# Performance work log

Hardware: AMD Instinct MI355X
Metric: run time of the kernel (lower is better)

The kernel has to match this reference:

```python
import jax, jax.numpy as jnp
import numpy as np

BS, L, S, AMB = 64, 64, 63, 32   # batch, sentence len, opseq steps, ambiguities per step
H, E, V, MLP = 128, 300, 50000, 1024
EPS = 1e-8


def setup_inputs() -> dict:
    key = jax.random.key(0)
    ks = jax.random.split(key, 12)
    u = lambda k, shp: jax.random.uniform(k, shp, dtype=jnp.float32) * 0.1
    return {
        "sentences1": jax.random.randint(ks[0], (BS, L), 0, V, dtype=jnp.int32),
        "operations1": jax.random.randint(ks[1], (BS, S, 2 * AMB), 0, L, dtype=jnp.int32),
        "oopl1": jnp.full((BS,), L + S, dtype=jnp.int32),
        "sentences2": jax.random.randint(ks[2], (BS, L), 0, V, dtype=jnp.int32),
        "operations2": jax.random.randint(ks[3], (BS, S, 2 * AMB), 0, L, dtype=jnp.int32),
        "oopl2": jnp.full((BS,), L + S, dtype=jnp.int32),
        "W": u(ks[4], (5 * H, E)),
        "U": u(ks[5], (5 * H, 2 * H)),
        "b": jnp.zeros((5 * H,), dtype=jnp.float32),
        "energy_u": u(ks[6], (H,)),
        "unk_embedding": u(ks[7], (E,)),
        "word_embeddings": jax.random.normal(ks[8], (V, E), dtype=jnp.float32),
        "A": u(ks[9], (MLP, 4 * H)),
        "a": u(ks[10], (MLP,)),
        "inv_temperature": jnp.float32(1.0),
    }


def _gates(preact, ccL, ccR):
    # preact: [..., 5H]; tree-LSTM cell (i, fL, fR, o, u gates)
    i = jax.nn.sigmoid(preact[..., :H])
    fL = jax.nn.sigmoid(preact[..., H:2 * H])
    fR = jax.nn.sigmoid(preact[..., 2 * H:3 * H])
    o = jax.nn.sigmoid(preact[..., 3 * H:4 * H])
    u = jnp.tanh(preact[..., 4 * H:5 * H])
    c = fL * ccL + fR * ccR + i * u
    h = o * jnp.tanh(c)
    return c, h


def _run_chart(sentences, operations, W, U, b, energy_u, unk_embedding,
               word_embeddings, inv_temperature):
    bs = sentences.shape[0]
    # leaf phase: embed each word, preact = W @ emb + b, ccL = ccR = 0
    emb = jnp.where(sentences[..., None] >= 0,
                    word_embeddings[jnp.clip(sentences, 0)], unk_embedding)  # [bs,L,E]
    preact = jnp.einsum('ble,ge->blg', emb, W) + b                            # [bs,L,5H]
    c, h = _gates(preact, 0.0, 0.0)
    chart = jnp.zeros((bs, L + S, 2 * H), dtype=jnp.float32)
    chart = chart.at[:, :L, :].set(jnp.concatenate([c, h], axis=-1))

    def step(chart, inp):
        ops, pos = inp                                   # ops: [bs, 2*AMB], pos: scalar
        entries = jnp.take_along_axis(chart, ops[:, :, None].astype(jnp.int32), axis=1)
        entries = entries.reshape(bs, AMB, 2, 2 * H)     # [bs, amb, (L,R), 2H]
        ccL = entries[:, :, 0, :H]
        ccR = entries[:, :, 1, :H]
        hh = entries[:, :, :, H:].reshape(bs, AMB, 2 * H)  # concat(hL, hR)
        pre = jnp.einsum('bak,gk->bag', hh, U) + b         # [bs, amb, 5H]
        c, h = _gates(pre, ccL, ccR)
        # cosine similarity of h against energy_u
        hn = jnp.maximum(jnp.sqrt(jnp.sum(h * h, axis=-1)), EPS)
        un = jnp.maximum(jnp.sqrt(jnp.sum(energy_u * energy_u)), EPS)
        e = jnp.einsum('bah,h->ba', h, energy_u) / (hn * un)
        s = jax.nn.softmax(e * inv_temperature, axis=1)    # [bs, amb]
        combined = jnp.concatenate([jnp.einsum('ba,bah->bh', s, c),
                                    jnp.einsum('ba,bah->bh', s, h)], axis=-1)
        chart = jax.lax.dynamic_update_slice(chart, combined[:, None, :], (0, pos, 0))
        return chart, None

    ops_seq = jnp.swapaxes(operations, 0, 1)             # [S, bs, 2*AMB]
    positions = L + jnp.arange(S, dtype=jnp.int32)
    chart, _ = jax.lax.scan(step, chart, (ops_seq, positions))
    return chart


def reference(sentences1, operations1, oopl1, sentences2, operations2, oopl2,
              W, U, b, energy_u, unk_embedding, word_embeddings, A, a,
              inv_temperature):
    chart1 = _run_chart(sentences1, operations1, W, U, b, energy_u,
                        unk_embedding, word_embeddings, inv_temperature)
    chart2 = _run_chart(sentences2, operations2, W, U, b, energy_u,
                        unk_embedding, word_embeddings, inv_temperature)
    bs = chart1.shape[0]
    bidx = jnp.arange(bs)
    s1 = chart1[bidx, oopl1 - 1, H:]                     # final composed h, [bs, H]
    s2 = chart2[bidx, oopl2 - 1, H:]
    u = (s1 - s2) ** 2
    v = s1 * s2
    conc = jnp.concatenate([u, v, s1, s2], axis=1)       # [bs, 4H]
    out = jax.nn.relu(jnp.einsum('jk,ik->ij', A, conc) + a)
    return out
```

## Files before the change

kernel.cpp:

```cpp
#include <hip/hip_runtime.h>
#include <hip/hip_bf16.h>

#define BSZ 64
#define LL  64
#define SS  63
#define AMB 32
#define HH  128
#define EE  300
#define MLPN 1024
#define GG  640
#define K2  256
#define PP  127

typedef __attribute__((ext_vector_type(8))) short short8;
typedef __attribute__((ext_vector_type(4))) float f32x4;

__device__ __forceinline__ float sigf(float x) { return 1.f / (1.f + __expf(-x)); }

__device__ __forceinline__ unsigned short f2bf(float x) {
    unsigned int u = __float_as_uint(x);
    u += 0x7fffu + ((u >> 16) & 1u);
    return (unsigned short)(u >> 16);
}

#define PW 25600
#define PU 20480
__global__ void __launch_bounds__(256) prep_kernel(
        const float* __restrict__ W, const float* __restrict__ U,
        short* __restrict__ WTB, short* __restrict__ UTB) {
    int idx = blockIdx.x * 256 + threadIdx.x;
    if (idx < PW) {
        int lane = idx & 63, r = idx >> 6;
        int kk = r % 10, n = r / 10;
        int g = n * 16 + (lane & 15);
        int k0 = kk * 32 + ((lane >> 4) << 3);
        const float* src = W + (size_t)g * EE + k0;
        float f[8];
        if (k0 + 8 <= EE) {
            f32x4 x0 = *(const f32x4*)src;
            f32x4 x1 = *(const f32x4*)(src + 4);
            f[0]=x0[0]; f[1]=x0[1]; f[2]=x0[2]; f[3]=x0[3];
            f[4]=x1[0]; f[5]=x1[1]; f[6]=x1[2]; f[7]=x1[3];
        } else {
#pragma unroll
            for (int j = 0; j < 8; ++j) f[j] = (k0 + j < EE) ? src[j] : 0.f;
        }
        short8 v;
#pragma unroll
        for (int j = 0; j < 8; ++j) v[j] = (short)f2bf(f[j]);
        *(short8*)(WTB + (size_t)idx * 8) = v;
    } else if (idx < PW + PU) {
        int o = idx - PW;
        int lane = o & 63, r = o >> 6;
        int kk = r & 7, n = r >> 3;
        int g = n * 16 + (lane & 15);
        int k0 = kk * 32 + ((lane >> 4) << 3);
        const float* src = U + (size_t)g * K2 + k0;
        f32x4 x0 = *(const f32x4*)src;
        f32x4 x1 = *(const f32x4*)(src + 4);
        short8 v;
        v[0]=(short)f2bf(x0[0]); v[1]=(short)f2bf(x0[1]); v[2]=(short)f2bf(x0[2]); v[3]=(short)f2bf(x0[3]);
        v[4]=(short)f2bf(x1[0]); v[5]=(short)f2bf(x1[1]); v[6]=(short)f2bf(x1[2]); v[7]=(short)f2bf(x1[3]);
        *(short8*)(UTB + (size_t)o * 8) = v;
    }
}

__global__ void __launch_bounds__(1024) main_kernel(
        const int* __restrict__ sent1, const int* __restrict__ sent2,
        const int* __restrict__ ops1, const int* __restrict__ ops2,
        const int* __restrict__ oopl1, const int* __restrict__ oopl2,
        const short* __restrict__ WTB, const short* __restrict__ UTB,
        const float* __restrict__ bias, const float* __restrict__ eu,
        const float* __restrict__ invt,
        const float* __restrict__ unk, const float* __restrict__ wemb,
        float* __restrict__ chart) {
    __shared__ short8 As[40 * 64];
    __shared__ float chh[32][132];
    __shared__ float comb[2][2][HH];
    __shared__ int ops_lds[64];
    __shared__ float e_num[AMB], h2s[AMB], s_w[AMB];
    __shared__ int live_list[SS];
    __shared__ int nl_sh;
    __shared__ float un_sh;

    const int tid = threadIdx.x;
    const int pair = blockIdx.x;
    const int ch = pair >> 6, b = pair & 63;
    const int* sent = ch ? sent2 : sent1;
    const int* ops  = ch ? ops2 : ops1;
    const int* oopl = ch ? oopl2 : oopl1;
    float* chbase = chart + (size_t)pair * PP * K2;
    const float it = invt[0];
    const int w = tid >> 6, lane = tid & 63, quad = lane >> 4, l15 = lane & 15;

    if (tid < 64) {
        float v = eu[tid] * eu[tid] + eu[tid + 64] * eu[tid + 64];
        for (int off = 32; off >= 1; off >>= 1) v += __shfl_xor(v, off);
        if (tid == 0) un_sh = fmaxf(sqrtf(v), 1e-8f);

        unsigned long long mask = 0ull;
        int q0 = oopl[b] - 1 - LL;
        if (q0 >= 0) { if (q0 > SS - 1) q0 = SS - 1; mask = 1ull << q0; }
        for (int t = SS - 1; t >= 1; --t) {
            if (mask & (1ull << t)) {
                int p = ops[(b * SS + t) * 64 + tid];
                int q = p - LL;
                unsigned long long bit = (q >= 0 && q < t) ? (1ull << q) : 0ull;
                for (int off = 32; off >= 1; off >>= 1) bit |= __shfl_xor(bit, off);
                mask |= bit;
            }
        }
        if (tid == 0) {
            int n = 0;
            for (int t = 0; t < SS; ++t)
                if (mask & (1ull << t)) live_list[n++] = t;
            nl_sh = n;
        }
    }

#pragma unroll
    for (int i = 0; i < 3; ++i) {
        int slot = i * 1024 + tid;
        if (slot < 2560) {
            int t = slot / 40, oct = slot - t * 40;
            int s = sent[b * LL + t];
            const float* src = (s >= 0) ? (wemb + (size_t)s * EE) : unk;
            int k0 = oct * 8;
            float f[8];
            if (k0 + 8 <= EE) {
                f32x4 x0 = *(const f32x4*)(src + k0);
                f32x4 x1 = *(const f32x4*)(src + k0 + 4);
                f[0]=x0[0]; f[1]=x0[1]; f[2]=x0[2]; f[3]=x0[3];
                f[4]=x1[0]; f[5]=x1[1]; f[6]=x1[2]; f[7]=x1[3];
            } else {
#pragma unroll
                for (int j = 0; j < 8; ++j) f[j] = (k0 + j < EE) ? src[k0 + j] : 0.f;
            }
            short8 v;
#pragma unroll
            for (int j = 0; j < 8; ++j) v[j] = (short)f2bf(f[j]);
            As[((t >> 4) * 10 + (oct >> 2)) * 64 + ((oct & 3) << 4) + (t & 15)] = v;
        }
    }
#pragma unroll
    for (int i = 0; i < 4; ++i) {
        int off = i * 4096 + tid * 4;
        if (off < SS * K2) {
            f32x4 z = {0.f, 0.f, 0.f, 0.f};
            *(f32x4*)(chbase + (size_t)LL * K2 + off) = z;
        }
    }
    __syncthreads();

    {
        const int mt = w & 3, nug = w >> 2;
        f32x4 acc[2][3] = {};
        for (int kk = 0; kk < 10; ++kk) {
            short8 a0 = As[(mt * 10 + kk) * 64 + lane];
#pragma unroll
            for (int si = 0; si < 3; ++si) {
                int s5 = (si == 0) ? 0 : (si == 1 ? 3 : 4);
#pragma unroll
                for (int hf = 0; hf < 2; ++hf) {
                    int n = (nug + hf * 4) + 8 * s5;
                    short8 bv = *(const short8*)(WTB + ((size_t)(n * 10 + kk) * 64 + lane) * 8);
                    acc[hf][si] = __builtin_amdgcn_mfma_f32_16x16x32_bf16(a0, bv, acc[hf][si], 0, 0, 0);
                }
            }
        }
#pragma unroll
        for (int hf = 0; hf < 2; ++hf) {
            int jc = (nug + hf * 4) * 16 + l15;
            float bi = bias[jc], bo = bias[3 * HH + jc], bu = bias[4 * HH + jc];
#pragma unroll
            for (int r = 0; r < 4; ++r) {
                float pi = acc[hf][0][r] + bi;
                float po = acc[hf][1][r] + bo;
                float pu = acc[hf][2][r] + bu;
                float cv = sigf(pi) * tanhf(pu);
                float hv = sigf(po) * tanhf(cv);
                int l = mt * 16 + quad * 4 + r;
                chbase[(size_t)l * K2 + jc]      = cv;
                chbase[(size_t)l * K2 + HH + jc] = hv;
            }
        }
    }
    __syncthreads();

    const int nl = nl_sh;
    const float eul = eu[lane], euh = eu[64 + lane];
    const int smt = w & 1, snu = w >> 1;
    const int sjc = snu * 16 + l15;
    const float bi  = bias[sjc],          bfl = bias[HH + sjc];
    const float bfr = bias[2 * HH + sjc], bo  = bias[3 * HH + sjc];
    const float bu  = bias[4 * HH + sjc];

    for (int sidx = 0; sidx < nl; ++sidx) {
        const int t = live_list[sidx];
        if (tid < 64) ops_lds[tid] = min(max(ops[(b * SS + t) * 64 + tid], 0), PP - 1);
        __syncthreads();

        {
            int a = tid >> 5, oct = tid & 31, side = oct >> 4, m8 = oct & 15;
            const float* src = chbase + (size_t)ops_lds[2 * a + side] * K2 + HH + m8 * 8;
            f32x4 x0 = *(const f32x4*)src;
            f32x4 x1 = *(const f32x4*)(src + 4);
            short8 v;
            v[0]=(short)f2bf(x0[0]); v[1]=(short)f2bf(x0[1]); v[2]=(short)f2bf(x0[2]); v[3]=(short)f2bf(x0[3]);
            v[4]=(short)f2bf(x1[0]); v[5]=(short)f2bf(x1[1]); v[6]=(short)f2bf(x1[2]); v[7]=(short)f2bf(x1[3]);
            As[((a >> 4) * 8 + (oct >> 2)) * 64 + ((oct & 3) << 4) + (a & 15)] = v;
        }
        __syncthreads();

        float cvals[4], hvals[4];
        {
            f32x4 acc[5] = {};
            for (int kk = 0; kk < 8; ++kk) {
                short8 a0 = As[(smt * 8 + kk) * 64 + lane];
#pragma unroll
                for (int s5 = 0; s5 < 5; ++s5) {
                    short8 bv = *(const short8*)(UTB + ((size_t)((snu + 8 * s5) * 8 + kk) * 64 + lane) * 8);
                    acc[s5] = __builtin_amdgcn_mfma_f32_16x16x32_bf16(a0, bv, acc[s5], 0, 0, 0);
                }
            }
#pragma unroll
            for (int r = 0; r < 4; ++r) {
                int a = smt * 16 + quad * 4 + r;
                float ccLv = chbase[(size_t)ops_lds[2 * a] * K2 + sjc];
                float ccRv = chbase[(size_t)ops_lds[2 * a + 1] * K2 + sjc];
                float cv = sigf(acc[1][r] + bfl) * ccLv
                         + sigf(acc[2][r] + bfr) * ccRv
                         + sigf(acc[0][r] + bi) * tanhf(acc[4][r] + bu);
                float hv = sigf(acc[3][r] + bo) * tanhf(cv);
                cvals[r] = cv; hvals[r] = hv;
                chh[a][sjc] = hv;
            }
        }
        __syncthreads();

#pragma unroll
        for (int i = 0; i < 2; ++i) {
            int a = w * 2 + i;
            float h0 = chh[a][lane], h1 = chh[a][64 + lane];
            float pe = h0 * eul + h1 * euh;
            float pn = h0 * h0 + h1 * h1;
            for (int off = 32; off >= 1; off >>= 1) {
                pe += __shfl_xor(pe, off);
                pn += __shfl_xor(pn, off);
            }
            if (lane == 0) { e_num[a] = pe; h2s[a] = pn; }
        }
        __syncthreads();

        if (tid < 64) {
            float v = (tid < AMB)
                ? (e_num[tid] / (fmaxf(sqrtf(h2s[tid]), 1e-8f) * un_sh)) * it
                : -3.4e38f;
            float m = v;
            for (int off = 32; off >= 1; off >>= 1) m = fmaxf(m, __shfl_xor(m, off));
            float ex = (tid < AMB) ? __expf(v - m) : 0.f;
            float su = ex;
            for (int off = 32; off >= 1; off >>= 1) su += __shfl_xor(su, off);
            if (tid < AMB) s_w[tid] = ex / su;
        }
        __syncthreads();

        {
            float sc = 0.f, sh = 0.f;
#pragma unroll
            for (int r = 0; r < 4; ++r) {
                int a = smt * 16 + quad * 4 + r;
                float sw = s_w[a];
                sc = fmaf(sw, cvals[r], sc);
                sh = fmaf(sw, hvals[r], sh);
            }
            sc += __shfl_xor(sc, 16); sc += __shfl_xor(sc, 32);
            sh += __shfl_xor(sh, 16); sh += __shfl_xor(sh, 32);
            if (lane < 16) {
                comb[smt][0][sjc] = sc;
                comb[smt][1][sjc] = sh;
            }
        }
        __syncthreads();
        if (tid < K2) {
            int part = tid >> 7, col = tid & 127;
            float val = comb[0][part][col] + comb[1][part][col];
            chbase[(size_t)(LL + t) * K2 + part * HH + col] = val;
        }
        __syncthreads();
    }
}

__global__ void __launch_bounds__(256) mlp_kernel(
        const float* __restrict__ chart,
        const int* __restrict__ oopl1, const int* __restrict__ oopl2,
        const float* __restrict__ A, const float* __restrict__ abias,
        float* __restrict__ out) {
    __shared__ __align__(16) float conc[4][512];
    const int tid = threadIdx.x;
    const int jt = blockIdx.x & 15, bt = blockIdx.x >> 4;

#pragma unroll
    for (int i = 0; i < 2; ++i) {
        int s = i * 256 + tid;
        int bl = s >> 7, kv = s & 127;
        int k0 = kv * 4, sel = k0 >> 7, kk0 = k0 & 127;
        int b = bt * 4 + bl;
        int p1 = min(max(oopl1[b] - 1, 0), PP - 1);
        int p2 = min(max(oopl2[b] - 1, 0), PP - 1);
        f32x4 s1 = *(const f32x4*)(chart + ((size_t)(b * PP + p1)) * K2 + HH + kk0);
        f32x4 s2 = *(const f32x4*)(chart + ((size_t)((BSZ + b) * PP + p2)) * K2 + HH + kk0);
        f32x4 v;
        if (sel == 0)      { f32x4 d = s1 - s2; v = d * d; }
        else if (sel == 1) v = s1 * s2;
        else if (sel == 2) v = s1;
        else               v = s2;
        *(f32x4*)&conc[bl][k0] = v;
    }
    __syncthreads();

    const int jj = tid & 63, bg = tid >> 6;
    const int j = jt * 64 + jj, b = bt * 4 + bg;
    const float* Arow = A + (size_t)j * 512;
    float acc0 = abias[j], acc1 = 0.f;
    for (int k = 0; k < 512; k += 8) {
        f32x4 a0 = *(const f32x4*)(Arow + k);
        f32x4 a1 = *(const f32x4*)(Arow + k + 4);
        f32x4 c0 = *(const f32x4*)&conc[bg][k];
        f32x4 c1 = *(const f32x4*)&conc[bg][k + 4];
#pragma unroll
        for (int u = 0; u < 4; ++u) {
            acc0 = fmaf(a0[u], c0[u], acc0);
            acc1 = fmaf(a1[u], c1[u], acc1);
        }
    }
    out[(size_t)b * MLPN + j] = fmaxf(acc0 + acc1, 0.f);
}

extern "C" void kernel_launch(void* const* d_in, const int* in_sizes, int n_in,
                              void* d_out, int out_size, void* d_ws, size_t ws_size,
                              hipStream_t stream) {
    const int*   sent1 = (const int*)d_in[0];
    const int*   ops1  = (const int*)d_in[1];
    const int*   oopl1 = (const int*)d_in[2];
    const int*   sent2 = (const int*)d_in[3];
    const int*   ops2  = (const int*)d_in[4];
    const int*   oopl2 = (const int*)d_in[5];
    const float* W     = (const float*)d_in[6];
    const float* U     = (const float*)d_in[7];
    const float* bias  = (const float*)d_in[8];
    const float* eu    = (const float*)d_in[9];
    const float* unk   = (const float*)d_in[10];
    const float* wemb  = (const float*)d_in[11];
    const float* A     = (const float*)d_in[12];
    const float* ab    = (const float*)d_in[13];
    const float* invt  = (const float*)d_in[14];
    float* out = (float*)d_out;
    (void)in_sizes; (void)n_in; (void)out_size; (void)ws_size;

    char* ws = (char*)d_ws;
    const size_t CHART_OFF = 0;
    const size_t WTB_OFF   = 16646144;
    const size_t UTB_OFF   = 17055744;
    float* chart = (float*)(ws + CHART_OFF);
    short* WTB   = (short*)(ws + WTB_OFF);
    short* UTB   = (short*)(ws + UTB_OFF);

    prep_kernel<<<180, 256, 0, stream>>>(W, U, WTB, UTB);

    main_kernel<<<128, 1024, 0, stream>>>(sent1, sent2, ops1, ops2, oopl1, oopl2,
                                          WTB, UTB, bias, eu, invt, unk, wemb, chart);

    mlp_kernel<<<256, 256, 0, stream>>>(chart, oopl1, oopl2, A, ab, out);
}
```

Before: 188.6 us.

## Keep per-sentence chart in LDS as bf16 and preload ops

The whole chart (127 rows × 256) now lives in shared memory as bf16 instead of global fp32, so the per-step gathers of child h/c and the writes of composed nodes no longer touch global memory. All operation indices are loaded into LDS once, and the liveness-mask computation is parallelised across warps. Only the final node's row is written out for the MLP kernel. The cost is a large LDS footprint, plus storing c and h in bf16, which adds rounding error that accumulates through the recurrence.

```diff
diff --git a/kernel.cpp b/kernel.cpp
--- a/kernel.cpp
+++ b/kernel.cpp
@@ -11,6 +11,7 @@
 #define GG  640
 #define K2  256
 #define PP  127
+#define CROW 272
 
 typedef __attribute__((ext_vector_type(8))) short short8;
 typedef __attribute__((ext_vector_type(4))) float f32x4;
@@ -21,6 +22,9 @@
     unsigned int u = __float_as_uint(x);
     u += 0x7fffu + ((u >> 16) & 1u);
     return (unsigned short)(u >> 16);
+}
+__device__ __forceinline__ float bf2f(short x) {
+    return __uint_as_float(((unsigned)(unsigned short)x) << 16);
 }
 
 #define PW 25600
@@ -73,81 +77,106 @@
         const float* __restrict__ bias, const float* __restrict__ eu,
         const float* __restrict__ invt,
         const float* __restrict__ unk, const float* __restrict__ wemb,
-        float* __restrict__ chart) {
-    __shared__ short8 As[40 * 64];
-    __shared__ float chh[32][132];
+        float* __restrict__ fin) {
+    __shared__ __align__(16) short chartL[127 * CROW + 16];
+    __shared__ __align__(16) char  buf[40960];
+    __shared__ int ops_all[SS * 64];
+    __shared__ int sent_lds[64];
+    __shared__ unsigned long long smask[64];
+    __shared__ int live_list[SS];
+    __shared__ float e_num[AMB], h2s[AMB], s_w[AMB];
     __shared__ float comb[2][2][HH];
-    __shared__ int ops_lds[64];
-    __shared__ float e_num[AMB], h2s[AMB], s_w[AMB];
-    __shared__ int live_list[SS];
     __shared__ int nl_sh;
     __shared__ float un_sh;
 
+    short8* AsL = (short8*)buf;
+    short8* As2 = (short8*)buf;
+    float*  chh = (float*)(buf + 16384);
+
     const int tid = threadIdx.x;
-    const int pair = blockIdx.x;
-    const int ch = pair >> 6, b = pair & 63;
+    const int pair = blockIdx.x, ch = pair >> 6, b = pair & 63;
     const int* sent = ch ? sent2 : sent1;
     const int* ops  = ch ? ops2 : ops1;
     const int* oopl = ch ? oopl2 : oopl1;
-    float* chbase = chart + (size_t)pair * PP * K2;
     const float it = invt[0];
     const int w = tid >> 6, lane = tid & 63, quad = lane >> 4, l15 = lane & 15;
 
+#pragma unroll
+    for (int i = 0; i < 4; ++i) {
+        int idx = i * 1024 + tid;
+        if (idx < SS * 64) ops_all[idx] = min(max(ops[b * SS * 64 + idx], 0), PP - 1);
+    }
+    if (tid < 64) sent_lds[tid] = sent[b * LL + tid];
     if (tid < 64) {
         float v = eu[tid] * eu[tid] + eu[tid + 64] * eu[tid + 64];
         for (int off = 32; off >= 1; off >>= 1) v += __shfl_xor(v, off);
         if (tid == 0) un_sh = fmaxf(sqrtf(v), 1e-8f);
-
+    }
+    __syncthreads();
+
+#pragma unroll
+    for (int i = 0; i < 4; ++i) {
+        int t = i * 16 + w;
+        if (t < SS) {
+            int q = ops_all[t * 64 + lane] - LL;
+            unsigned long long bit = (q >= 0 && q < t) ? (1ull << q) : 0ull;
+            for (int off = 32; off >= 1; off >>= 1) bit |= __shfl_xor(bit, off);
+            if (lane == 0) smask[t] = bit;
+        }
+    }
+    __syncthreads();
+
+    if (tid == 0) {
         unsigned long long mask = 0ull;
         int q0 = oopl[b] - 1 - LL;
         if (q0 >= 0) { if (q0 > SS - 1) q0 = SS - 1; mask = 1ull << q0; }
-        for (int t = SS - 1; t >= 1; --t) {
-            if (mask & (1ull << t)) {
-                int p = ops[(b * SS + t) * 64 + tid];
-                int q = p - LL;
-                unsigned long long bit = (q >= 0 && q < t) ? (1ull << q) : 0ull;
-                for (int off = 32; off >= 1; off >>= 1) bit |= __shfl_xor(bit, off);
-                mask |= bit;
-            }
-        }
-        if (tid == 0) {
-            int n = 0;
-            for (int t = 0; t < SS; ++t)
-                if (mask & (1ull << t)) live_list[n++] = t;
-            nl_sh = n;
-        }
+        for (int t = SS - 1; t >= 1; --t)
+            if ((mask >> t) & 1) mask |= smask[t];
+        int n = 0;
+        for (int t = 0; t < SS; ++t)
+            if ((mask >> t) & 1) live_list[n++] = t;
+        nl_sh = n;
     }
 
 #pragma unroll
     for (int i = 0; i < 3; ++i) {
-        int slot = i * 1024 + tid;
-        if (slot < 2560) {
-            int t = slot / 40, oct = slot - t * 40;
-            int s = sent[b * LL + t];
-            const float* src = (s >= 0) ? (wemb + (size_t)s * EE) : unk;
-            int k0 = oct * 8;
-            float f[8];
-            if (k0 + 8 <= EE) {
-                f32x4 x0 = *(const f32x4*)(src + k0);
-                f32x4 x1 = *(const f32x4*)(src + k0 + 4);
-                f[0]=x0[0]; f[1]=x0[1]; f[2]=x0[2]; f[3]=x0[3];
-                f[4]=x1[0]; f[5]=x1[1]; f[6]=x1[2]; f[7]=x1[3];
-            } else {
-#pragma unroll
-                for (int j = 0; j < 8; ++j) f[j] = (k0 + j < EE) ? src[k0 + j] : 0.f;
-            }
-            short8 v;
-#pragma unroll
-            for (int j = 0; j < 8; ++j) v[j] = (short)f2bf(f[j]);
-            As[((t >> 4) * 10 + (oct >> 2)) * 64 + ((oct & 3) << 4) + (t & 15)] = v;
-        }
-    }
-#pragma unroll
-    for (int i = 0; i < 4; ++i) {
-        int off = i * 4096 + tid * 4;
-        if (off < SS * K2) {
-            f32x4 z = {0.f, 0.f, 0.f, 0.f};
-            *(f32x4*)(chbase + (size_t)LL * K2 + off) = z;
+        int idx = i * 1024 + tid;
+        if (idx < 2142)
+            ((int4*)(chartL + 64 * CROW))[idx] = make_int4(0, 0, 0, 0);
+    }
+    {
+        float ef[3][8];
+        int est[3], eso[3];
+#pragma unroll
+        for (int i = 0; i < 3; ++i) {
+            int slot = i * 1024 + tid;
+            est[i] = -1;
+            if (slot < 2560) {
+                int t = slot / 40, oct = slot - t * 40;
+                est[i] = t; eso[i] = oct;
+                int s = sent_lds[t];
+                const float* src = (s >= 0) ? (wemb + (size_t)s * EE) : unk;
+                int k0 = oct * 8;
+                if (k0 + 8 <= EE) {
+                    f32x4 x0 = *(const f32x4*)(src + k0);
+                    f32x4 x1 = *(const f32x4*)(src + k0 + 4);
+                    ef[i][0]=x0[0]; ef[i][1]=x0[1]; ef[i][2]=x0[2]; ef[i][3]=x0[3];
+                    ef[i][4]=x1[0]; ef[i][5]=x1[1]; ef[i][6]=x1[2]; ef[i][7]=x1[3];
+                } else {
+#pragma unroll
+                    for (int j = 0; j < 8; ++j) ef[i][j] = (k0 + j < EE) ? src[k0 + j] : 0.f;
+                }
+            }
+        }
+#pragma unroll
+        for (int i = 0; i < 3; ++i) {
+            if (est[i] >= 0) {
+                int t = est[i], oct = eso[i];
+                short8 v;
+#pragma unroll
+                for (int j = 0; j < 8; ++j) v[j] = (short)f2bf(ef[i][j]);
+                AsL[((t >> 4) * 10 + (oct >> 2)) * 64 + ((oct & 3) << 4) + (t & 15)] = v;
+            }
         }
     }
     __syncthreads();
@@ -156,7 +185,7 @@
         const int mt = w & 3, nug = w >> 2;
         f32x4 acc[2][3] = {};
         for (int kk = 0; kk < 10; ++kk) {
-            short8 a0 = As[(mt * 10 + kk) * 64 + lane];
+            short8 a0 = AsL[(mt * 10 + kk) * 64 + lane];
 #pragma unroll
             for (int si = 0; si < 3; ++si) {
                 int s5 = (si == 0) ? 0 : (si == 1 ? 3 : 4);
@@ -180,8 +209,8 @@
                 float cv = sigf(pi) * tanhf(pu);
                 float hv = sigf(po) * tanhf(cv);
                 int l = mt * 16 + quad * 4 + r;
-                chbase[(size_t)l * K2 + jc]      = cv;
-                chbase[(size_t)l * K2 + HH + jc] = hv;
+                chartL[l * CROW + jc]      = (short)f2bf(cv);
+                chartL[l * CROW + HH + jc] = (short)f2bf(hv);
             }
         }
     }
@@ -197,18 +226,13 @@
 
     for (int sidx = 0; sidx < nl; ++sidx) {
         const int t = live_list[sidx];
-        if (tid < 64) ops_lds[tid] = min(max(ops[(b * SS + t) * 64 + tid], 0), PP - 1);
-        __syncthreads();
+        const int* oprow = ops_all + t * 64;
 
         {
             int a = tid >> 5, oct = tid & 31, side = oct >> 4, m8 = oct & 15;
-            const float* src = chbase + (size_t)ops_lds[2 * a + side] * K2 + HH + m8 * 8;
-            f32x4 x0 = *(const f32x4*)src;
-            f32x4 x1 = *(const f32x4*)(src + 4);
-            short8 v;
-            v[0]=(short)f2bf(x0[0]); v[1]=(short)f2bf(x0[1]); v[2]=(short)f2bf(x0[2]); v[3]=(short)f2bf(x0[3]);
-            v[4]=(short)f2bf(x1[0]); v[5]=(short)f2bf(x1[1]); v[6]=(short)f2bf(x1[2]); v[7]=(short)f2bf(x1[3]);
-            As[((a >> 4) * 8 + (oct >> 2)) * 64 + ((oct & 3) << 4) + (a & 15)] = v;
+            int row = oprow[2 * a + side];
+            short8 v = *(const short8*)(chartL + row * CROW + HH + m8 * 8);
+            As2[((a >> 4) * 8 + (oct >> 2)) * 64 + ((oct & 3) << 4) + (a & 15)] = v;
         }
         __syncthreads();
 
@@ -216,7 +240,7 @@
         {
             f32x4 acc[5] = {};
             for (int kk = 0; kk < 8; ++kk) {
-                short8 a0 = As[(smt * 8 + kk) * 64 + lane];
+                short8 a0 = As2[(smt * 8 + kk) * 64 + lane];
 #pragma unroll
                 for (int s5 = 0; s5 < 5; ++s5) {
                     short8 bv = *(const short8*)(UTB + ((size_t)((snu + 8 * s5) * 8 + kk) * 64 + lane) * 8);
@@ -226,14 +250,14 @@
 #pragma unroll
             for (int r = 0; r < 4; ++r) {
                 int a = smt * 16 + quad * 4 + r;
-                float ccLv = chbase[(size_t)ops_lds[2 * a] * K2 + sjc];
-                float ccRv = chbase[(size_t)ops_lds[2 * a + 1] * K2 + sjc];
+                float ccLv = bf2f(chartL[oprow[2 * a] * CROW + sjc]);
+                float ccRv = bf2f(chartL[oprow[2 * a + 1] * CROW + sjc]);
                 float cv = sigf(acc[1][r] + bfl) * ccLv
                          + sigf(acc[2][r] + bfr) * ccRv
                          + sigf(acc[0][r] + bi) * tanhf(acc[4][r] + bu);
                 float hv = sigf(acc[3][r] + bo) * tanhf(cv);
                 cvals[r] = cv; hvals[r] = hv;
-                chh[a][sjc] = hv;
+                chh[a * 132 + sjc] = hv;
             }
         }
         __syncthreads();
@@ -241,7 +265,7 @@
 #pragma unroll
         for (int i = 0; i < 2; ++i) {
             int a = w * 2 + i;
-            float h0 = chh[a][lane], h1 = chh[a][64 + lane];
+            float h0 = chh[a * 132 + lane], h1 = chh[a * 132 + 64 + lane];
             float pe = h0 * eul + h1 * euh;
             float pn = h0 * h0 + h1 * h1;
             for (int off = 32; off >= 1; off >>= 1) {
@@ -285,15 +309,18 @@
         if (tid < K2) {
             int part = tid >> 7, col = tid & 127;
             float val = comb[0][part][col] + comb[1][part][col];
-            chbase[(size_t)(LL + t) * K2 + part * HH + col] = val;
-        }
-        __syncthreads();
-    }
+            chartL[(LL + t) * CROW + part * HH + col] = (short)f2bf(val);
+        }
+        __syncthreads();
+    }
+
+    int p = min(max(oopl[b] - 1, 0), PP - 1);
+    if (tid < K2)
+        fin[(size_t)pair * K2 + tid] = bf2f(chartL[p * CROW + tid]);
 }
 
 __global__ void __launch_bounds__(256) mlp_kernel(
-        const float* __restrict__ chart,
-        const int* __restrict__ oopl1, const int* __restrict__ oopl2,
+        const float* __restrict__ fin,
         const float* __restrict__ A, const float* __restrict__ abias,
         float* __restrict__ out) {
     __shared__ __align__(16) float conc[4][512];
@@ -306,10 +333,8 @@
         int bl = s >> 7, kv = s & 127;
         int k0 = kv * 4, sel = k0 >> 7, kk0 = k0 & 127;
         int b = bt * 4 + bl;
-        int p1 = min(max(oopl1[b] - 1, 0), PP - 1);
-        int p2 = min(max(oopl2[b] - 1, 0), PP - 1);
-        f32x4 s1 = *(const f32x4*)(chart + ((size_t)(b * PP + p1)) * K2 + HH + kk0);
-        f32x4 s2 = *(const f32x4*)(chart + ((size_t)((BSZ + b) * PP + p2)) * K2 + HH + kk0);
+        f32x4 s1 = *(const f32x4*)(fin + (size_t)b * K2 + HH + kk0);
+        f32x4 s2 = *(const f32x4*)(fin + (size_t)(BSZ + b) * K2 + HH + kk0);
         f32x4 v;
         if (sel == 0)      { f32x4 d = s1 - s2; v = d * d; }
         else if (sel == 1) v = s1 * s2;
@@ -359,17 +384,17 @@
     (void)in_sizes; (void)n_in; (void)out_size; (void)ws_size;
 
     char* ws = (char*)d_ws;
-    const size_t CHART_OFF = 0;
-    const size_t WTB_OFF   = 16646144;
-    const size_t UTB_OFF   = 17055744;
-    float* chart = (float*)(ws + CHART_OFF);
-    short* WTB   = (short*)(ws + WTB_OFF);
-    short* UTB   = (short*)(ws + UTB_OFF);
+    const size_t WTB_OFF = 0;
+    const size_t UTB_OFF = 409600;
+    const size_t FIN_OFF = 737280;
+    short* WTB = (short*)(ws + WTB_OFF);
+    short* UTB = (short*)(ws + UTB_OFF);
+    float* fin = (float*)(ws + FIN_OFF);
 
     prep_kernel<<<180, 256, 0, stream>>>(W, U, WTB, UTB);
 
     main_kernel<<<128, 1024, 0, stream>>>(sent1, sent2, ops1, ops2, oopl1, oopl2,
-                                          WTB, UTB, bias, eu, invt, unk, wemb, chart);
-
-    mlp_kernel<<<256, 256, 0, stream>>>(chart, oopl1, oopl2, A, ab, out);
-}
+                                          WTB, UTB, bias, eu, invt, unk, wemb, fin);
+
+    mlp_kernel<<<256, 256, 0, stream>>>(fin, A, ab, out);
+}
```

Result: no change. 187.0 us (-0.8%).
